# Kernel tuning notes

Measured on AMD Instinct MI355X. Metric: run time of the kernel, lower is better.

## Reference

```python
import jax, jax.numpy as jnp
import numpy as np

EMB_DIM, TREE_DIM, OUT_DIM, VOCAB = 256, 256, 3, 10000
T, B, LEVELS = 255, 128, 8  # complete binary tree of depth 8, 128 trees per input


def _build_forest():
    # node j = T-1-heap(j): root (heap 0) is the LAST node so stack_last_h picks the root.
    heap = np.arange(T)
    depth = np.floor(np.log2(heap + 1)).astype(np.int64)  # 0..7
    node_order = np.empty(T, dtype=np.int64)
    node_order[T - 1 - heap] = (LEVELS - 1) - depth       # leaves=0, root=7
    internal = np.arange((T - 1) // 2)                     # heaps with two children
    parent = np.repeat(T - 1 - internal, 2)
    child = np.stack([T - 1 - (2 * internal + 1), T - 1 - (2 * internal + 2)], 1).reshape(-1)
    edges = np.stack([parent, child], axis=1)              # (254, 2)
    edge_order = node_order[parent]
    offs = (np.arange(B) * T)[:, None, None]
    adj = (edges[None] + offs).reshape(-1, 2)              # (B*254, 2)
    return np.tile(node_order, B), adj, np.tile(edge_order, B)


def setup_inputs() -> dict:
    key = jax.random.key(0)
    ks = jax.random.split(key, 16)
    no, adj, eo = _build_forest()
    D = TREE_DIM
    s_e = 1.0 / np.sqrt(EMB_DIM)
    s_t = 1.0 / np.sqrt(D)
    return {
        'feat_cube': jax.random.randint(ks[0], (B * T,), 0, VOCAB),
        'feat_a': jax.random.randint(ks[1], (B * T,), 0, VOCAB),
        'feat_b': jax.random.randint(ks[2], (B * T,), 0, VOCAB),
        'node_order': jnp.asarray(no),
        'adjacency_list': jnp.asarray(adj),
        'edge_order': jnp.asarray(eo),
        'num_levels': LEVELS,
        'num_trees': B,
        'emb': jax.random.normal(ks[3], (VOCAB, EMB_DIM), jnp.float32),
        'W_iou': jax.random.normal(ks[4], (3 * D, EMB_DIM), jnp.float32) * s_e,
        'b_iou': jnp.zeros((3 * D,), jnp.float32),
        'U_iou': jax.random.normal(ks[5], (3 * D, D), jnp.float32) * s_t,
        'W_f': jax.random.normal(ks[6], (D, EMB_DIM), jnp.float32) * s_e,
        'b_f': jnp.zeros((D,), jnp.float32),
        'U_f': jax.random.normal(ks[7], (D, D), jnp.float32) * s_t,
        'fc1_w': jax.random.normal(ks[8], (D // 2, D), jnp.float32) * s_t,
        'fc1_b': jnp.zeros((D // 2,), jnp.float32),
        'fc2_w': jax.random.normal(ks[9], (OUT_DIM, D // 2), jnp.float32) * (1.0 / np.sqrt(D // 2)),
        'fc2_b': jnp.zeros((OUT_DIM,), jnp.float32),
    }


def _tree_lstm(x, node_order, parents, children, edge_order, W_iou, b_iou, U_iou, W_f, b_f, U_f, num_levels):
    # Child-sum TreeLSTM, evaluated level by level (leaves first). Dense masked
    # formulation: per level we update only nodes with node_order==lvl; edge
    # contributions are masked before segment_sum (same math as the torch loop).
    N = x.shape[0]
    D = U_f.shape[0]
    x_iou = x @ W_iou.T + b_iou            # (N, 3D), precomputed once
    x_f = x @ W_f.T + b_f                  # (N, D)
    h = jnp.zeros((N, D), x.dtype)
    c = jnp.zeros((N, D), x.dtype)
    for lvl in range(num_levels):
        emask = (edge_order == lvl)[:, None].astype(x.dtype)
        ch = h[children]                   # (E, D) gather of child hidden
        cc = c[children]
        f = jax.nn.sigmoid(x_f[parents] + ch @ U_f.T)
        h_sum = jax.ops.segment_sum(ch * emask, parents, num_segments=N)
        c_sum = jax.ops.segment_sum(f * cc * emask, parents, num_segments=N)
        i, o, u = jnp.split(x_iou + h_sum @ U_iou.T, 3, axis=1)
        c_new = jax.nn.sigmoid(i) * jnp.tanh(u) + c_sum
        h_new = jax.nn.sigmoid(o) * jnp.tanh(c_new)
        nmask = (node_order == lvl)[:, None]
        h = jnp.where(nmask, h_new, h)
        c = jnp.where(nmask, c_new, c)
    return h, c


def reference(feat_cube, feat_a, feat_b, node_order, adjacency_list, edge_order,
              num_levels, num_trees, emb, W_iou, b_iou, U_iou, W_f, b_f, U_f,
              fc1_w, fc1_b, fc2_w, fc2_b):
    parents = adjacency_list[:, 0]
    children = adjacency_list[:, 1]

    def run_tree(feat):
        h, _ = _tree_lstm(emb[feat], node_order, parents, children, edge_order,
                          W_iou, b_iou, U_iou, W_f, b_f, U_f, num_levels)
        # stack_last_h: last node of each tree (= root with our labeling)
        return h.reshape(num_trees, -1, h.shape[-1])[:, -1, :]

    h_c = run_tree(feat_cube)
    h_a = run_tree(feat_a)
    h_b = run_tree(feat_b)
    # h_c (1,D) @ (h_a (D,1) @ h_b (1,D)) == (h_c . h_a) * h_b, fused einsum
    h = jnp.einsum('bi,bi,bj->bj', h_c, h_a, h_b)
    hid = jax.nn.relu(h @ fc1_w.T + fc1_b)
    logits = jax.nn.relu(hid @ fc2_w.T + fc2_b)
    return logits  # (num_trees, out_dim)
```

## Files before the change

### kernel.cpp

```cpp
#include <hip/hip_runtime.h>
#include <hip/hip_bf16.h>

typedef __hip_bfloat16 bf16;
typedef unsigned short u16;
typedef __attribute__((ext_vector_type(8))) short s8;
typedef __attribute__((ext_vector_type(4))) float f4;

#define NRUNS 3
#define NTREE 128
#define TT    255
#define DD    256
#define VPAD  10016
#define PAD   258
#define OPAD  264
#define FPAD  264

__device__ __forceinline__ float bits2f(u16 b){ union{unsigned u; float f;} x; x.u = ((unsigned)b)<<16; return x.f; }
__device__ __forceinline__ u16   f2bits(float f){ bf16 h = __float2bfloat16(f); return *(u16*)&h; }
__device__ __forceinline__ float sigm(float x){ return 1.f/(1.f+__expf(-x)); }
__device__ __forceinline__ float tanh_(float x){ return 1.f - 2.f/(__expf(2.f*x)+1.f); }

__global__ void k_detect(const u16* __restrict__ raw, int* __restrict__ flag){
    int t = threadIdx.x;
    int hit = 0;
    if (t < 128){
        u16 w = raw[2*t];
        int e = (w >> 7) & 0xFF;
        hit = (e >= 100 && e <= 141) ? 1 : 0;
    }
    __shared__ int cnt;
    if (t == 0) cnt = 0;
    __syncthreads();
    atomicAdd(&cnt, hit);
    __syncthreads();
    if (t == 0) flag[0] = (cnt >= 64) ? 1 : 0;
}

__device__ __forceinline__ u16 cvt1b(const void* p, int i, int isb){
    return isb ? ((const u16*)p)[i] : f2bits(((const float*)p)[i]);
}
__device__ __forceinline__ float cvt1f(const void* p, int i, int isb){
    return isb ? bits2f(((const u16*)p)[i]) : ((const float*)p)[i];
}

#define L_EMB  (10000*256)
#define L_EMBP (VPAD*256)
#define L_WIOU (768*256)
#define L_UIOU (768*256)
#define L_WF   (256*256)
#define L_UF   (256*256)
#define L_ALL  (L_EMBP + L_WIOU + L_UIOU + L_WF + L_UF)
__global__ void k_cvtb(const void* __restrict__ s0, const void* __restrict__ s1,
                       const void* __restrict__ s2, const void* __restrict__ s3,
                       const void* __restrict__ s4,
                       u16* __restrict__ d0, u16* __restrict__ d1, u16* __restrict__ d2,
                       u16* __restrict__ d3, u16* __restrict__ d4,
                       const int* __restrict__ flag){
    int isb = flag[0];
    for (int i = blockIdx.x*blockDim.x + threadIdx.x; i < L_ALL; i += gridDim.x*blockDim.x){
        int j = i;
        if (j < L_EMBP){ d0[j] = (j < L_EMB) ? cvt1b(s0, j, isb) : (u16)0; continue; } j -= L_EMBP;
        if (j < L_WIOU){ d1[j] = cvt1b(s1, j, isb); continue; } j -= L_WIOU;
        if (j < L_UIOU){ d2[j] = cvt1b(s2, j, isb); continue; } j -= L_UIOU;
        if (j < L_WF){ d3[j] = cvt1b(s3, j, isb); continue; } j -= L_WF;
        d4[j] = cvt1b(s4, j, isb);
    }
}

#define S_BIOU 768
#define S_BF   256
#define S_F1W  (128*256)
#define S_F1B  128
#define S_F2W  (3*128)
#define S_F2B  3
#define S_ALL  (S_BIOU+S_BF+S_F1W+S_F1B+S_F2W+S_F2B)
__global__ void k_small(const void* __restrict__ s0, const void* __restrict__ s1,
                        const void* __restrict__ s2, const void* __restrict__ s3,
                        const void* __restrict__ s4, const void* __restrict__ s5,
                        float* __restrict__ d0, float* __restrict__ d1, float* __restrict__ d2,
                        float* __restrict__ d3, float* __restrict__ d4, float* __restrict__ d5,
                        const int* __restrict__ flag){
    int isb = flag[0];
    for (int i = blockIdx.x*blockDim.x + threadIdx.x; i < S_ALL; i += gridDim.x*blockDim.x){
        int j = i;
        if (j < S_BIOU){ d0[j] = cvt1f(s0, j, isb); continue; } j -= S_BIOU;
        if (j < S_BF){ d1[j] = cvt1f(s1, j, isb); continue; } j -= S_BF;
        if (j < S_F1W){ d2[j] = cvt1f(s2, j, isb); continue; } j -= S_F1W;
        if (j < S_F1B){ d3[j] = cvt1f(s3, j, isb); continue; } j -= S_F1B;
        if (j < S_F2W){ d4[j] = cvt1f(s4, j, isb); continue; } j -= S_F2W;
        d5[j] = cvt1f(s5, j, isb);
    }
}

__device__ __forceinline__ s8 ldB16(const u16* p){
    union { uint4 q; s8 v; } u;
    u.q = *(const uint4*)p;
    return u.v;
}
__device__ __forceinline__ s8 ldsA(const u16* p){
    union { unsigned w[4]; s8 v; } u;
    u.w[0] = *(const unsigned*)(p);
    u.w[1] = *(const unsigned*)(p+2);
    u.w[2] = *(const unsigned*)(p+4);
    u.w[3] = *(const unsigned*)(p+6);
    return u.v;
}
#define MFMA(acc,a,b) acc = __builtin_amdgcn_mfma_f32_16x16x32_bf16(a, b, acc, 0, 0, 0)

__global__ __launch_bounds__(512, 4)
void k_vocab2(const u16* __restrict__ embb,
              const u16* __restrict__ Wiou, const u16* __restrict__ Wfm,
              const u16* __restrict__ Ufm,  const float* __restrict__ biou_f,
              u16* __restrict__ E4, u16* __restrict__ E_f,
              u16* __restrict__ H0, u16* __restrict__ C0, u16* __restrict__ HU0)
{
    __shared__ u16 hs[32*PAD];
    const int t = threadIdx.x, w = t>>6, lane = t&63, ln = lane&15, q = lane>>4;
    const int r0 = blockIdx.x*32, d0 = w*32;

    const u16* Bp[8];
    #pragma unroll
    for (int g = 0; g < 4; g++)
      #pragma unroll
      for (int nc = 0; nc < 2; nc++){
        int nn = d0 + nc*16 + ln;
        Bp[g*2+nc] = (g < 3) ? (Wiou + (size_t)(g*256+nn)*DD) : (Wfm + (size_t)nn*DD);
      }
    const u16* a0p = embb + (size_t)(r0+ln)*DD;
    const u16* a1p = embb + (size_t)(r0+16+ln)*DD;
    f4 acc[8][2];
    #pragma unroll
    for (int nt = 0; nt < 8; nt++){ acc[nt][0] = (f4){0,0,0,0}; acc[nt][1] = (f4){0,0,0,0}; }
    #pragma unroll 2
    for (int ks = 0; ks < 8; ks++){
        int ko = ks*32 + q*8;
        s8 a0 = ldB16(a0p + ko);
        s8 a1 = ldB16(a1p + ko);
        #pragma unroll
        for (int nt = 0; nt < 8; nt++){
            s8 bb = ldB16(Bp[nt] + ko);
            MFMA(acc[nt][0], a0, bb);
            MFMA(acc[nt][1], a1, bb);
        }
    }
    #pragma unroll
    for (int nc = 0; nc < 2; nc++){
        int d = d0 + nc*16 + ln;
        float bi = biou_f[d], bo = biou_f[256+d], bu = biou_f[512+d];
        #pragma unroll
        for (int ms = 0; ms < 2; ms++)
          #pragma unroll
          for (int r = 0; r < 4; r++){
            int vrow = r0 + ms*16 + q*4 + r;
            float ei = acc[0*2+nc][ms][r];
            float eo = acc[1*2+nc][ms][r];
            float eu = acc[2*2+nc][ms][r];
            float ef = acc[3*2+nc][ms][r];
            union { u16 a[4]; uint2 q2; } pk;
            pk.a[0] = f2bits(ei);
            pk.a[1] = f2bits(eo);
            pk.a[2] = f2bits(eu);
            pk.a[3] = f2bits(ef);
            *(uint2*)(E4 + ((size_t)vrow*DD + d)*4) = pk.q2;
            E_f[(size_t)vrow*DD + d] = f2bits(ef);
            float cc = sigm(ei + bi)*tanh_(eu + bu);
            float hh = sigm(eo + bo)*tanh_(cc);
            C0[(size_t)vrow*DD + d] = f2bits(cc);
            H0[(size_t)vrow*DD + d] = f2bits(hh);
            hs[(ms*16 + q*4 + r)*PAD + d] = f2bits(hh);
        }
    }
    __syncthreads();

    f4 hacc[2][2];
    #pragma unroll
    for (int nt = 0; nt < 2; nt++){ hacc[nt][0] = (f4){0,0,0,0}; hacc[nt][1] = (f4){0,0,0,0}; }
    const u16* Bf0 = Ufm + (size_t)(d0 + ln)*DD;
    const u16* Bf1 = Ufm + (size_t)(d0 + 16 + ln)*DD;
    #pragma unroll 2
    for (int ks = 0; ks < 8; ks++){
        int ko = ks*32 + q*8;
        s8 a0 = ldsA(&hs[ln*PAD + ko]);
        s8 a1 = ldsA(&hs[(16+ln)*PAD + ko]);
        s8 b0 = ldB16(Bf0 + ko);
        s8 b1 = ldB16(Bf1 + ko);
        MFMA(hacc[0][0], a0, b0); MFMA(hacc[0][1], a1, b0);
        MFMA(hacc[1][0], a0, b1); MFMA(hacc[1][1], a1, b1);
    }
    #pragma unroll
    for (int nc = 0; nc < 2; nc++){
        int d = d0 + nc*16 + ln;
        #pragma unroll
        for (int ms = 0; ms < 2; ms++)
          #pragma unroll
          for (int r = 0; r < 4; r++){
            int vrow = r0 + ms*16 + q*4 + r;
            HU0[(size_t)vrow*DD + d] = f2bits(hacc[nc][ms][r]);
        }
    }
}

__global__ __launch_bounds__(512, 4)
void k_edge0(const int* __restrict__ f0, const int* __restrict__ f1, const int* __restrict__ f2,
             const u16* __restrict__ E_f, const u16* __restrict__ H0,
             const u16* __restrict__ C0,  const u16* __restrict__ HU0,
             const float* __restrict__ bf_f,
             u16* __restrict__ hsum_out, u16* __restrict__ fcsum_out)
{
    int gid = blockIdx.x*512 + threadIdx.x;
    int row = gid >> 5, ch = gid & 31, d = ch*8;
    int run = row >> 13, rem = row & 8191, b = rem >> 6, jj = rem & 63;
    const int* fp = (run==0) ? f0 : ((run==1) ? f1 : f2);
    int fo = fp[b*TT + 128 + jj];
    int v1 = fp[b*TT + 2*jj];
    int v2 = fp[b*TT + 2*jj + 1];
    s8 ef  = ldB16(E_f + (size_t)fo*DD + d);
    s8 hu1 = ldB16(HU0 + (size_t)v1*DD + d);
    s8 hu2 = ldB16(HU0 + (size_t)v2*DD + d);
    s8 c1  = ldB16(C0  + (size_t)v1*DD + d);
    s8 c2  = ldB16(C0  + (size_t)v2*DD + d);
    s8 h1  = ldB16(H0  + (size_t)v1*DD + d);
    s8 h2  = ldB16(H0  + (size_t)v2*DD + d);
    union { u16 a[8]; uint4 q4; } uh, uf;
    #pragma unroll
    for (int j = 0; j < 8; j++){
        float e  = bits2f((u16)ef[j]) + bf_f[d+j];
        float fa = sigm(e + bits2f((u16)hu1[j]));
        float fb = sigm(e + bits2f((u16)hu2[j]));
        float fc = fa*bits2f((u16)c1[j]) + fb*bits2f((u16)c2[j]);
        float hsv = bits2f((u16)h1[j]) + bits2f((u16)h2[j]);
        uf.a[j] = f2bits(fc);
        uh.a[j] = f2bits(hsv);
    }
    *(uint4*)(hsum_out  + (size_t)row*DD + d) = uh.q4;
    *(uint4*)(fcsum_out + (size_t)row*DD + d) = uf.q4;
}

__global__ __launch_bounds__(512, 4)
void k_lvl(int lvl, int cLog,
           const int* __restrict__ f0, const int* __restrict__ f1, const int* __restrict__ f2,
           const u16* __restrict__ E4, const u16* __restrict__ E_f,
           const u16* __restrict__ Uiou, const u16* __restrict__ Ufm,
           const float* __restrict__ biou_f, const float* __restrict__ bf_f,
           const u16* __restrict__ hsum_in, const u16* __restrict__ fcsum_in,
           u16* __restrict__ hsum_out, u16* __restrict__ fcsum_out,
           u16* __restrict__ hroot)
{
    __shared__ u16 hs[32*PAD];
    __shared__ u16 hso[16*OPAD];
    __shared__ u16 fco[16*OPAD];
    __shared__ int sfr[32];
    const int t = threadIdx.x, w = t>>6, lane = t&63, ln = lane&15, q = lane>>4;
    const int cnt = 1 << cLog, S = 256 - 2*cnt;
    const int r0 = blockIdx.x*32, d0 = w*32;
    const bool haveP = (lvl < 7);

    if (t < 32){
        int rho = r0 + t;
        int run = rho >> (7+cLog);
        int rem = rho & ((1<<(7+cLog)) - 1);
        int b = rem >> cLog, jj = rem & (cnt-1);
        const int* fp = (run==0) ? f0 : ((run==1) ? f1 : f2);
        sfr[t] = fp[b*TT + S + jj];
    }

    int featp[2][2];
    if (haveP){
        #pragma unroll
        for (int ms = 0; ms < 2; ms++)
          #pragma unroll
          for (int rr = 0; rr < 2; rr++){
            int rho = r0 + ms*16 + q*4 + rr*2;
            int run = rho >> (7+cLog);
            int rem = rho & ((1<<(7+cLog)) - 1);
            int b = rem >> cLog, jj = rem & (cnt-1);
            const int* fp = (run==0) ? f0 : ((run==1) ? f1 : f2);
            featp[ms][rr] = fp[b*TT + (256-cnt) + (jj>>1)];
          }
    }
    __syncthreads();

    f4 acc[6][2];
    #pragma unroll
    for (int nt = 0; nt < 6; nt++){ acc[nt][0] = (f4){0,0,0,0}; acc[nt][1] = (f4){0,0,0,0}; }
    {
        const u16* a0p = hsum_in + (size_t)(r0+ln)*DD;
        const u16* a1p = hsum_in + (size_t)(r0+16+ln)*DD;
        const u16* Bp[6];
        #pragma unroll
        for (int nt = 0; nt < 6; nt++){
            int n = (nt>>1)*256 + d0 + (nt&1)*16 + ln;
            Bp[nt] = Uiou + (size_t)n*DD;
        }
        #pragma unroll 2
        for (int ks = 0; ks < 8; ks++){
            int ko = ks*32 + q*8;
            s8 a0 = ldB16(a0p + ko);
            s8 a1 = ldB16(a1p + ko);
            #pragma unroll
            for (int nt = 0; nt < 6; nt++){
                s8 bb = ldB16(Bp[nt] + ko);
                MFMA(acc[nt][0], a0, bb);
                MFMA(acc[nt][1], a1, bb);
            }
        }
    }

    float cv[2][2][4];
    #pragma unroll
    for (int nc = 0; nc < 2; nc++){
        int d = d0 + nc*16 + ln;
        float bi = biou_f[d], bo = biou_f[256+d], bu = biou_f[512+d];
        #pragma unroll
        for (int ms = 0; ms < 2; ms++){
            float hv[4];
            #pragma unroll
            for (int r = 0; r < 4; r++){
                int m   = ms*16 + q*4 + r;
                int rho = r0 + m;
                union { uint2 q2; u16 a[4]; } ev;
                ev.q2 = *(const uint2*)(E4 + ((size_t)sfr[m]*DD + d)*4);
                float iv = acc[0+nc][ms][r] + bits2f(ev.a[0]) + bi;
                float ov = acc[2+nc][ms][r] + bits2f(ev.a[1]) + bo;
                float uv = acc[4+nc][ms][r] + bits2f(ev.a[2]) + bu;
                float cs = bits2f(fcsum_in[(size_t)rho*DD + d]);
                float c = sigm(iv)*tanh_(uv) + cs;
                float h = sigm(ov)*tanh_(c);
                cv[nc][ms][r] = c;
                hv[r] = h;
                if (haveP) hs[m*PAD + d] = f2bits(h);
                else       hroot[(size_t)rho*DD + d] = f2bits(h);
            }
            if (haveP){
                int lr = ms*8 + q*2;
                hso[lr*OPAD + d]     = f2bits(hv[0] + hv[1]);
                hso[(lr+1)*OPAD + d] = f2bits(hv[2] + hv[3]);
            }
        }
    }

    if (haveP){
        __syncthreads();
        f4 hacc[2][2];
        #pragma unroll
        for (int nt = 0; nt < 2; nt++){ hacc[nt][0] = (f4){0,0,0,0}; hacc[nt][1] = (f4){0,0,0,0}; }
        const u16* Bf0 = Ufm + (size_t)(d0 + ln)*DD;
        const u16* Bf1 = Ufm + (size_t)(d0 + 16 + ln)*DD;
        #pragma unroll 2
        for (int ks = 0; ks < 8; ks++){
            int ko = ks*32 + q*8;
            s8 a0 = ldsA(&hs[ln*PAD + ko]);
            s8 a1 = ldsA(&hs[(16+ln)*PAD + ko]);
            s8 b0 = ldB16(Bf0 + ko);
            s8 b1 = ldB16(Bf1 + ko);
            MFMA(hacc[0][0], a0, b0); MFMA(hacc[0][1], a1, b0);
            MFMA(hacc[1][0], a0, b1); MFMA(hacc[1][1], a1, b1);
        }
        #pragma unroll
        for (int nc = 0; nc < 2; nc++){
            int d = d0 + nc*16 + ln;
            float bfv = bf_f[d];
            #pragma unroll
            for (int ms = 0; ms < 2; ms++){
                float fs0, fs1;
                #pragma unroll
                for (int r = 0; r < 4; r++){
                    float ef = bits2f(E_f[(size_t)featp[ms][r>>1]*DD + d]);
                    float fc = sigm(ef + bfv + hacc[nc][ms][r]) * cv[nc][ms][r];
                    if (r == 0) fs0 = fc;
                    else if (r == 1) fs0 += fc;
                    else if (r == 2) fs1 = fc;
                    else fs1 += fc;
                }
                int lr = ms*8 + q*2;
                fco[lr*OPAD + d]     = f2bits(fs0);
                fco[(lr+1)*OPAD + d] = f2bits(fs1);
            }
        }

        __syncthreads();
        {
            int row = t >> 5, c = (t & 31) * 8;
            int prow = (r0 >> 1) + row;
            uint4 vh = *(const uint4*)&hso[row*OPAD + c];
            uint4 vf = *(const uint4*)&fco[row*OPAD + c];
            *(uint4*)(hsum_out  + (size_t)prow*DD + c) = vh;
            *(uint4*)(fcsum_out + (size_t)prow*DD + c) = vf;
        }
    }
}

__global__ __launch_bounds__(512, 2)
void k_tail(const int* __restrict__ f0, const int* __restrict__ f1, const int* __restrict__ f2,
            const u16* __restrict__ E4, const u16* __restrict__ E_f,
            const u16* __restrict__ Uiou, const u16* __restrict__ Ufm,
            const float* __restrict__ biou_f, const float* __restrict__ bf_f,
            const u16* __restrict__ hsum_in, const u16* __restrict__ fcsum_in,
            u16* __restrict__ hroot)
{
    __shared__ u16 hs[32*PAD];
    __shared__ u16 hsP[2][32*PAD];
    __shared__ u16 fcP[2][32*FPAD];
    __shared__ int sf[64];
    const int t = threadIdx.x, w = t>>6, lane = t&63, ln = lane&15, q = lane>>4;
    const int d0 = w*32;
    const int r0 = blockIdx.x*32;
    const int run = (blockIdx.x*4) >> 7;
    const int* __restrict__ fp = (run==0) ? f0 : ((run==1) ? f1 : f2);

    if (t < 64){
        int ti = t >> 4, idx = t & 15;
        int b = (blockIdx.x*4 + ti) & 127;
        sf[t] = (idx < 15) ? fp[b*TT + 240 + idx] : 0;
    }
    __syncthreads();

    const u16* Bp[6];
    #pragma unroll
    for (int nt = 0; nt < 6; nt++){
        int n = (nt>>1)*256 + d0 + (nt&1)*16 + ln;
        Bp[nt] = Uiou + (size_t)n*DD;
    }
    const u16* Bf0 = Ufm + (size_t)(d0 + ln)*DD;
    const u16* Bf1 = Ufm + (size_t)(d0 + 16 + ln)*DD;

    for (int l = 4; l <= 7; l++){
        const int nl = 128 >> l;
        const int nrows = 4*nl;
        const int sh = 7 - l;
        const int inb = (l-1) & 1, outb = l & 1;
        const bool haveP = (l < 7);

        f4 acc[6][2];
        #pragma unroll
        for (int nt = 0; nt < 6; nt++){ acc[nt][0] = (f4){0,0,0,0}; acc[nt][1] = (f4){0,0,0,0}; }
        if (l == 4){
            const u16* a0p = hsum_in + (size_t)(r0+ln)*DD;
            const u16* a1p = hsum_in + (size_t)(r0+16+ln)*DD;
            #pragma unroll 2
            for (int ks = 0; ks < 8; ks++){
                int ko = ks*32 + q*8;
                s8 a0 = ldB16(a0p + ko);
                s8 a1 = ldB16(a1p + ko);
                #pragma unroll
                for (int nt = 0; nt < 6; nt++){
                    s8 bb = ldB16(Bp[nt] + ko);
                    MFMA(acc[nt][0], a0, bb);
                    MFMA(acc[nt][1], a1, bb);
                }
            }
        } else {
            const u16* a0l = &hsP[inb][ln*PAD];
            const u16* a1l = &hsP[inb][(16+ln)*PAD];
            #pragma unroll 2
            for (int ks = 0; ks < 8; ks++){
                int ko = ks*32 + q*8;
                s8 a0 = ldsA(a0l + ko);
                s8 a1 = ldsA(a1l + ko);
                #pragma unroll
                for (int nt = 0; nt < 6; nt++){
                    s8 bb = ldB16(Bp[nt] + ko);
                    MFMA(acc[nt][0], a0, bb);
                    MFMA(acc[nt][1], a1, bb);
                }
            }
        }

        float cv[2][2][4];
        #pragma unroll
        for (int nc = 0; nc < 2; nc++){
            int d = d0 + nc*16 + ln;
            float bi = biou_f[d], bo = biou_f[256+d], bu = biou_f[512+d];
            #pragma unroll
            for (int ms = 0; ms < 2; ms++){
                float hv[4];
                #pragma unroll
                for (int r = 0; r < 4; r++){
                    int m = ms*16 + q*4 + r;
                    bool vld = (m < nrows);
                    int mc = vld ? m : 0;
                    int ti = mc >> sh, jj = mc & (nl-1);
                    int fidx = sf[ti*16 + (16 - 2*nl) + jj];
                    union { uint2 q2; u16 a[4]; } ev;
                    ev.q2 = *(const uint2*)(E4 + ((size_t)fidx*DD + d)*4);
                    float iv = acc[0+nc][ms][r] + bits2f(ev.a[0]) + bi;
                    float ov = acc[2+nc][ms][r] + bits2f(ev.a[1]) + bo;
                    float uv = acc[4+nc][ms][r] + bits2f(ev.a[2]) + bu;
                    float cs = (l == 4) ? bits2f(fcsum_in[(size_t)(r0+m)*DD + d])
                                        : bits2f(fcP[inb][m*FPAD + d]);
                    float c = sigm(iv)*tanh_(uv) + cs;
                    float h = sigm(ov)*tanh_(c);
                    cv[nc][ms][r] = c;
                    hv[r] = h;
                    if (haveP) hs[m*PAD + d] = f2bits(h);
                    else if (vld) hroot[(size_t)(blockIdx.x*4 + m)*DD + d] = f2bits(h);
                }
                if (haveP){
                    int lr = ms*8 + q*2;
                    hsP[outb][lr*PAD + d]     = f2bits(hv[0] + hv[1]);
                    hsP[outb][(lr+1)*PAD + d] = f2bits(hv[2] + hv[3]);
                }
            }
        }

        if (haveP){
            __syncthreads();
            f4 hacc[2][2];
            #pragma unroll
            for (int nt = 0; nt < 2; nt++){ hacc[nt][0] = (f4){0,0,0,0}; hacc[nt][1] = (f4){0,0,0,0}; }
            #pragma unroll 2
            for (int ks = 0; ks < 8; ks++){
                int ko = ks*32 + q*8;
                s8 a0 = ldsA(&hs[ln*PAD + ko]);
                s8 a1 = ldsA(&hs[(16+ln)*PAD + ko]);
                s8 b0 = ldB16(Bf0 + ko);
                s8 b1 = ldB16(Bf1 + ko);
                MFMA(hacc[0][0], a0, b0); MFMA(hacc[0][1], a1, b0);
                MFMA(hacc[1][0], a0, b1); MFMA(hacc[1][1], a1, b1);
            }
            #pragma unroll
            for (int nc = 0; nc < 2; nc++){
                int d = d0 + nc*16 + ln;
                float bfv = bf_f[d];
                #pragma unroll
                for (int ms = 0; ms < 2; ms++){
                    float fs0, fs1;
                    #pragma unroll
                    for (int r = 0; r < 4; r++){
                        int m2 = ms*16 + q*4 + (r & 2);
                        int mc2 = (m2 < nrows) ? m2 : 0;
                        int ti2 = mc2 >> sh, jj2 = mc2 & (nl-1);
                        int fpar = sf[ti2*16 + (16 - nl) + (jj2 >> 1)];
                        float ef = bits2f(E_f[(size_t)fpar*DD + d]);
                        float fc = sigm(ef + bfv + hacc[nc][ms][r]) * cv[nc][ms][r];
                        if (r == 0) fs0 = fc;
                        else if (r == 1) fs0 += fc;
                        else if (r == 2) fs1 = fc;
                        else fs1 += fc;
                    }
                    int lr = ms*8 + q*2;
                    fcP[outb][lr*FPAD + d]     = f2bits(fs0);
                    fcP[outb][(lr+1)*FPAD + d] = f2bits(fs1);
                }
            }
            __syncthreads();
        }
    }
}

__global__ __launch_bounds__(256)
void k_final(const u16* __restrict__ hroot,
             const float* __restrict__ fc1w, const float* __restrict__ fc1b,
             const float* __restrict__ fc2w, const float* __restrict__ fc2b,
             void* __restrict__ out, const int* __restrict__ flag)
{
    int b = blockIdx.x, t = threadIdx.x;
    __shared__ float sprod[DD];
    __shared__ float shb[DD];
    __shared__ float shid[128];
    float hc  = bits2f(hroot[(0*NTREE + b)*DD + t]);
    float ha  = bits2f(hroot[(1*NTREE + b)*DD + t]);
    float hbv = bits2f(hroot[(2*NTREE + b)*DD + t]);
    sprod[t] = hc * ha;
    shb[t]   = hbv;
    __syncthreads();
    for (int s = 128; s > 0; s >>= 1){
        if (t < s) sprod[t] += sprod[t + s];
        __syncthreads();
    }
    float dot = sprod[0];
    if (t < 128){
        float acc = fc1b[t];
        for (int k = 0; k < DD; k++)
            acc = fmaf(dot * shb[k], fc1w[t*DD + k], acc);
        shid[t] = fmaxf(acc, 0.f);
    }
    __syncthreads();
    if (t < 3){
        float acc = fc2b[t];
        for (int j = 0; j < 128; j++)
            acc = fmaf(fc2w[t*128 + j], shid[j], acc);
        float v = fmaxf(acc, 0.f);
        if (flag[0]) ((bf16*)out)[b*3 + t] = __float2bfloat16(v);
        else         ((float*)out)[b*3 + t] = v;
    }
}

extern "C" void kernel_launch(void* const* d_in, const int* in_sizes, int n_in,
                              void* d_out, int out_size, void* d_ws, size_t ws_size,
                              hipStream_t stream)
{
    const int* f0 = (const int*)d_in[0];
    const int* f1 = (const int*)d_in[1];
    const int* f2 = (const int*)d_in[2];
    const void* emb  = d_in[8];
    const void* Wiou = d_in[9];
    const void* biou = d_in[10];
    const void* Uiou = d_in[11];
    const void* Wf   = d_in[12];
    const void* bfv  = d_in[13];
    const void* Uf   = d_in[14];
    const void* fc1w = d_in[15];
    const void* fc1b = d_in[16];
    const void* fc2w = d_in[17];
    const void* fc2b = d_in[18];

    char* base = (char*)d_ws;
    size_t off = 0;
    auto take = [&](size_t bytes) -> char* {
        char* p = base + off;
        off = (off + bytes + 255) & ~(size_t)255;
        return p;
    };
    int*   flag   = (int*)  take(256);
    u16*   embb   = (u16*)  take((size_t)L_EMBP*2);
    u16*   wioub  = (u16*)  take((size_t)L_WIOU*2);
    u16*   uioub  = (u16*)  take((size_t)L_UIOU*2);
    u16*   wfb    = (u16*)  take((size_t)L_WF*2);
    u16*   ufb    = (u16*)  take((size_t)L_UF*2);
    float* biou_f = (float*)take(S_BIOU*4);
    float* bf_f   = (float*)take(S_BF*4);
    float* fc1w_f = (float*)take(S_F1W*4);
    float* fc1b_f = (float*)take(S_F1B*4);
    float* fc2w_f = (float*)take(S_F2W*4);
    float* fc2b_f = (float*)take(S_F2B*4);
    u16*   E4     = (u16*)  take((size_t)VPAD*DD*4*2);
    u16*   E_f    = (u16*)  take((size_t)VPAD*DD*2);
    u16*   H0     = (u16*)  take((size_t)VPAD*DD*2);
    u16*   C0     = (u16*)  take((size_t)VPAD*DD*2);
    u16*   HU0    = (u16*)  take((size_t)VPAD*DD*2);
    u16*   HA     = (u16*)  take((size_t)24576*DD*2);
    u16*   HB     = (u16*)  take((size_t)12288*DD*2);
    u16*   FA     = (u16*)  take((size_t)24576*DD*2);
    u16*   FB     = (u16*)  take((size_t)12288*DD*2);
    u16*   hroot  = (u16*)  take((size_t)NRUNS*NTREE*DD*2);

    k_detect<<<1, 256, 0, stream>>>((const u16*)emb, flag);
    k_cvtb<<<2048, 256, 0, stream>>>(emb, Wiou, Uiou, Wf, Uf,
                                     embb, wioub, uioub, wfb, ufb, flag);
    k_small<<<135, 256, 0, stream>>>(biou, bfv, fc1w, fc1b, fc2w, fc2b,
                                     biou_f, bf_f, fc1w_f, fc1b_f, fc2w_f, fc2b_f, flag);
    k_vocab2<<<VPAD/32, 512, 0, stream>>>(embb, wioub, wfb, ufb, biou_f,
                                          E4, E_f, H0, C0, HU0);
    k_edge0<<<24576*32/512, 512, 0, stream>>>(f0, f1, f2, E_f, H0, C0, HU0, bf_f, HA, FA);

    for (int lvl = 1; lvl <= 3; lvl++){
        int cLog = 7 - lvl;
        int rows = NRUNS*NTREE*(128 >> lvl);
        int blocks = rows / 32;
        int pe = lvl & 1;
        u16* hs_o = pe ? HB : HA;
        u16* fc_o = pe ? FB : FA;
        const u16* hs_i = pe ? HA : HB;
        const u16* fc_i = pe ? FA : FB;
        k_lvl<<<blocks, 512, 0, stream>>>(lvl, cLog, f0, f1, f2,
                                          E4, E_f, uioub, ufb,
                                          biou_f, bf_f,
                                          hs_i, fc_i, hs_o, fc_o, hroot);
    }
    k_tail<<<(NRUNS*NTREE)/4, 512, 0, stream>>>(f0, f1, f2, E4, E_f, uioub, ufb,
                                                biou_f, bf_f, HB, FB, hroot);
    k_final<<<NTREE, 256, 0, stream>>>(hroot, fc1w_f, fc1b_f, fc2w_f, fc2b_f, d_out, flag);
}
```

Measured before the change: 431.2 us.

## Split k_tail work over 16 waves with 16 columns each and prefetch gathers

New measurement: 421.3 us. -2.3%, faster.

```diff
diff --git a/kernel.cpp b/kernel.cpp
--- a/kernel.cpp
+++ b/kernel.cpp
@@ -390,7 +390,7 @@
     }
 }
 
-__global__ __launch_bounds__(512, 2)
+__global__ __launch_bounds__(1024, 4)
 void k_tail(const int* __restrict__ f0, const int* __restrict__ f1, const int* __restrict__ f2,
             const u16* __restrict__ E4, const u16* __restrict__ E_f,
             const u16* __restrict__ Uiou, const u16* __restrict__ Ufm,
@@ -403,7 +403,8 @@
     __shared__ u16 fcP[2][32*FPAD];
     __shared__ int sf[64];
     const int t = threadIdx.x, w = t>>6, lane = t&63, ln = lane&15, q = lane>>4;
-    const int d0 = w*32;
+    const int d0 = w*16;
+    const int d  = d0 + ln;
     const int r0 = blockIdx.x*32;
     const int run = (blockIdx.x*4) >> 7;
     const int* __restrict__ fp = (run==0) ? f0 : ((run==1) ? f1 : f2);
@@ -415,14 +416,14 @@
     }
     __syncthreads();
 
-    const u16* Bp[6];
-    #pragma unroll
-    for (int nt = 0; nt < 6; nt++){
-        int n = (nt>>1)*256 + d0 + (nt&1)*16 + ln;
-        Bp[nt] = Uiou + (size_t)n*DD;
-    }
+    const u16* Bp[3];
+    #pragma unroll
+    for (int g = 0; g < 3; g++)
+        Bp[g] = Uiou + (size_t)(g*256 + d0 + ln)*DD;
     const u16* Bf0 = Ufm + (size_t)(d0 + ln)*DD;
-    const u16* Bf1 = Ufm + (size_t)(d0 + 16 + ln)*DD;
+
+    const float bi = biou_f[d], bo = biou_f[256+d], bu = biou_f[512+d];
+    const float bfv = bf_f[d];
 
     for (int l = 4; l <= 7; l++){
         const int nl = 128 >> l;
@@ -431,9 +432,9 @@
         const int inb = (l-1) & 1, outb = l & 1;
         const bool haveP = (l < 7);
 
-        f4 acc[6][2];
-        #pragma unroll
-        for (int nt = 0; nt < 6; nt++){ acc[nt][0] = (f4){0,0,0,0}; acc[nt][1] = (f4){0,0,0,0}; }
+        f4 acc[3][2];
+        #pragma unroll
+        for (int nt = 0; nt < 3; nt++){ acc[nt][0] = (f4){0,0,0,0}; acc[nt][1] = (f4){0,0,0,0}; }
         if (l == 4){
             const u16* a0p = hsum_in + (size_t)(r0+ln)*DD;
             const u16* a1p = hsum_in + (size_t)(r0+16+ln)*DD;
@@ -443,7 +444,7 @@
                 s8 a0 = ldB16(a0p + ko);
                 s8 a1 = ldB16(a1p + ko);
                 #pragma unroll
-                for (int nt = 0; nt < 6; nt++){
+                for (int nt = 0; nt < 3; nt++){
                     s8 bb = ldB16(Bp[nt] + ko);
                     MFMA(acc[nt][0], a0, bb);
                     MFMA(acc[nt][1], a1, bb);
@@ -458,7 +459,7 @@
                 s8 a0 = ldsA(a0l + ko);
                 s8 a1 = ldsA(a1l + ko);
                 #pragma unroll
-                for (int nt = 0; nt < 6; nt++){
+                for (int nt = 0; nt < 3; nt++){
                     s8 bb = ldB16(Bp[nt] + ko);
                     MFMA(acc[nt][0], a0, bb);
                     MFMA(acc[nt][1], a1, bb);
@@ -466,82 +467,88 @@
             }
         }
 
-        float cv[2][2][4];
-        #pragma unroll
-        for (int nc = 0; nc < 2; nc++){
-            int d = d0 + nc*16 + ln;
-            float bi = biou_f[d], bo = biou_f[256+d], bu = biou_f[512+d];
+        uint2 ev[2][4];
+        float csv[2][4];
+        #pragma unroll
+        for (int ms = 0; ms < 2; ms++)
+          #pragma unroll
+          for (int r = 0; r < 4; r++){
+            int m = ms*16 + q*4 + r;
+            int mc = (m < nrows) ? m : 0;
+            int ti = mc >> sh, jj = mc & (nl-1);
+            int fidx = sf[ti*16 + (16 - 2*nl) + jj];
+            ev[ms][r] = *(const uint2*)(E4 + ((size_t)fidx*DD + d)*4);
+            csv[ms][r] = (l == 4) ? bits2f(fcsum_in[(size_t)(r0+m)*DD + d])
+                                  : bits2f(fcP[inb][m*FPAD + d]);
+        }
+
+        float cv[2][4];
+        #pragma unroll
+        for (int ms = 0; ms < 2; ms++){
+            float hv[4];
             #pragma unroll
-            for (int ms = 0; ms < 2; ms++){
-                float hv[4];
-                #pragma unroll
-                for (int r = 0; r < 4; r++){
-                    int m = ms*16 + q*4 + r;
-                    bool vld = (m < nrows);
-                    int mc = vld ? m : 0;
-                    int ti = mc >> sh, jj = mc & (nl-1);
-                    int fidx = sf[ti*16 + (16 - 2*nl) + jj];
-                    union { uint2 q2; u16 a[4]; } ev;
-                    ev.q2 = *(const uint2*)(E4 + ((size_t)fidx*DD + d)*4);
-                    float iv = acc[0+nc][ms][r] + bits2f(ev.a[0]) + bi;
-                    float ov = acc[2+nc][ms][r] + bits2f(ev.a[1]) + bo;
-                    float uv = acc[4+nc][ms][r] + bits2f(ev.a[2]) + bu;
-                    float cs = (l == 4) ? bits2f(fcsum_in[(size_t)(r0+m)*DD + d])
-                                        : bits2f(fcP[inb][m*FPAD + d]);
-                    float c = sigm(iv)*tanh_(uv) + cs;
-                    float h = sigm(ov)*tanh_(c);
-                    cv[nc][ms][r] = c;
-                    hv[r] = h;
-                    if (haveP) hs[m*PAD + d] = f2bits(h);
-                    else if (vld) hroot[(size_t)(blockIdx.x*4 + m)*DD + d] = f2bits(h);
-                }
-                if (haveP){
-                    int lr = ms*8 + q*2;
-                    hsP[outb][lr*PAD + d]     = f2bits(hv[0] + hv[1]);
-                    hsP[outb][(lr+1)*PAD + d] = f2bits(hv[2] + hv[3]);
-                }
+            for (int r = 0; r < 4; r++){
+                int m = ms*16 + q*4 + r;
+                bool vld = (m < nrows);
+                union { uint2 q2; u16 a[4]; } u2;
+                u2.q2 = ev[ms][r];
+                float iv = acc[0][ms][r] + bits2f(u2.a[0]) + bi;
+                float ov = acc[1][ms][r] + bits2f(u2.a[1]) + bo;
+                float uv = acc[2][ms][r] + bits2f(u2.a[2]) + bu;
+                float c = sigm(iv)*tanh_(uv) + csv[ms][r];
+                float h = sigm(ov)*tanh_(c);
+                cv[ms][r] = c;
+                hv[r] = h;
+                if (haveP) hs[m*PAD + d] = f2bits(h);
+                else if (vld) hroot[(size_t)(blockIdx.x*4 + m)*DD + d] = f2bits(h);
+            }
+            if (haveP){
+                int lr = ms*8 + q*2;
+                hsP[outb][lr*PAD + d]     = f2bits(hv[0] + hv[1]);
+                hsP[outb][(lr+1)*PAD + d] = f2bits(hv[2] + hv[3]);
             }
         }
 
         if (haveP){
             __syncthreads();
-            f4 hacc[2][2];
-            #pragma unroll
-            for (int nt = 0; nt < 2; nt++){ hacc[nt][0] = (f4){0,0,0,0}; hacc[nt][1] = (f4){0,0,0,0}; }
+            f4 hacc[2];
+            hacc[0] = (f4){0,0,0,0}; hacc[1] = (f4){0,0,0,0};
             #pragma unroll 2
             for (int ks = 0; ks < 8; ks++){
                 int ko = ks*32 + q*8;
                 s8 a0 = ldsA(&hs[ln*PAD + ko]);
                 s8 a1 = ldsA(&hs[(16+ln)*PAD + ko]);
                 s8 b0 = ldB16(Bf0 + ko);
-                s8 b1 = ldB16(Bf1 + ko);
-                MFMA(hacc[0][0], a0, b0); MFMA(hacc[0][1], a1, b0);
-                MFMA(hacc[1][0], a0, b1); MFMA(hacc[1][1], a1, b1);
-            }
+                MFMA(hacc[0], a0, b0);
+                MFMA(hacc[1], a1, b0);
+            }
+
+            float efv[2][2];
             #pragma unroll
-            for (int nc = 0; nc < 2; nc++){
-                int d = d0 + nc*16 + ln;
-                float bfv = bf_f[d];
+            for (int ms = 0; ms < 2; ms++)
+              #pragma unroll
+              for (int rr = 0; rr < 2; rr++){
+                int m2 = ms*16 + q*4 + rr*2;
+                int mc2 = (m2 < nrows) ? m2 : 0;
+                int ti2 = mc2 >> sh, jj2 = mc2 & (nl-1);
+                int fpar = sf[ti2*16 + (16 - nl) + (jj2 >> 1)];
+                efv[ms][rr] = bits2f(E_f[(size_t)fpar*DD + d]);
+            }
+            #pragma unroll
+            for (int ms = 0; ms < 2; ms++){
+                float fs0, fs1;
                 #pragma unroll
-                for (int ms = 0; ms < 2; ms++){
-                    float fs0, fs1;
-                    #pragma unroll
-                    for (int r = 0; r < 4; r++){
-                        int m2 = ms*16 + q*4 + (r & 2);
-                        int mc2 = (m2 < nrows) ? m2 : 0;
-                        int ti2 = mc2 >> sh, jj2 = mc2 & (nl-1);
-                        int fpar = sf[ti2*16 + (16 - nl) + (jj2 >> 1)];
-                        float ef = bits2f(E_f[(size_t)fpar*DD + d]);
-                        float fc = sigm(ef + bfv + hacc[nc][ms][r]) * cv[nc][ms][r];
-                        if (r == 0) fs0 = fc;
-                        else if (r == 1) fs0 += fc;
-                        else if (r == 2) fs1 = fc;
-                        else fs1 += fc;
-                    }
-                    int lr = ms*8 + q*2;
-                    fcP[outb][lr*FPAD + d]     = f2bits(fs0);
-                    fcP[outb][(lr+1)*FPAD + d] = f2bits(fs1);
+                for (int r = 0; r < 4; r++){
+                    float ef = efv[ms][r>>1];
+                    float fc = sigm(ef + bfv + hacc[ms][r]) * cv[ms][r];
+                    if (r == 0) fs0 = fc;
+                    else if (r == 1) fs0 += fc;
+                    else if (r == 2) fs1 = fc;
+                    else fs1 += fc;
                 }
+                int lr = ms*8 + q*2;
+                fcP[outb][lr*FPAD + d]     = f2bits(fs0);
+                fcP[outb][(lr+1)*FPAD + d] = f2bits(fs1);
             }
             __syncthreads();
         }
@@ -658,7 +665,7 @@
                                           biou_f, bf_f,
                                           hs_i, fc_i, hs_o, fc_o, hroot);
     }
-    k_tail<<<(NRUNS*NTREE)/4, 512, 0, stream>>>(f0, f1, f2, E4, E_f, uioub, ufb,
-                                                biou_f, bf_f, HB, FB, hroot);
+    k_tail<<<(NRUNS*NTREE)/4, 1024, 0, stream>>>(f0, f1, f2, E4, E_f, uioub, ufb,
+                                                 biou_f, bf_f, HB, FB, hroot);
     k_final<<<NTREE, 256, 0, stream>>>(hroot, fc1w_f, fc1b_f, fc2w_f, fc2b_f, d_out, flag);
 }
```
